# Performance work log

Measured on AMD Instinct MI355X. Metric: run time of the kernel, lower is better.

## Reference

```python
import jax, jax.numpy as jnp
import numpy as np

MODEL_DIM = 1024
NUM_HEADS = 16
HEAD_DIM = MODEL_DIM // NUM_HEADS
WINDOW = 4


def local_mask(seq_len):
    i = jnp.arange(seq_len)
    return jnp.abs(i[:, None] - i[None, :]) <= WINDOW  # [S,S] bool


def setup_inputs() -> dict:
    key = jax.random.key(0)
    ks = jax.random.split(key, 9)
    d = MODEL_DIM
    s = 0.02
    return {
        "x": jax.random.normal(ks[0], (4, 2048, d), dtype=jnp.float32),
        "Wq": jax.random.normal(ks[1], (d, d), dtype=jnp.float32) * s,
        "bq": jnp.zeros((d,), dtype=jnp.float32),
        "Wk": jax.random.normal(ks[2], (d, d), dtype=jnp.float32) * s,
        "bk": jnp.zeros((d,), dtype=jnp.float32),
        "Wv": jax.random.normal(ks[3], (d, d), dtype=jnp.float32) * s,
        "bv": jnp.zeros((d,), dtype=jnp.float32),
        "Wo": jax.random.normal(ks[4], (d, d), dtype=jnp.float32) * s,
        "bo": jnp.zeros((d,), dtype=jnp.float32),
    }


def reference(x, Wq, bq, Wk, bk, Wv, bv, Wo, bo):
    B, S, D = x.shape
    H, Hd = NUM_HEADS, HEAD_DIM
    # linear projections (torch Linear: x @ W.T + b; here W stored pre-transposed)
    q = (x @ Wq + bq).reshape(B, S, H, Hd).transpose(0, 2, 1, 3)  # [B,H,S,Hd]
    k = (x @ Wk + bk).reshape(B, S, H, Hd).transpose(0, 2, 1, 3)
    v = (x @ Wv + bv).reshape(B, S, H, Hd).transpose(0, 2, 1, 3)
    scores = jnp.einsum("bhqd,bhkd->bhqk", q, k) / jnp.sqrt(jnp.float32(Hd))
    mask = local_mask(S)[None, None]  # [1,1,S,S]
    scores = jnp.where(mask, scores, -jnp.inf)
    weights = jax.nn.softmax(scores, axis=-1)  # [B,H,S,S]
    out = jnp.einsum("bhqk,bhkd->bhqd", weights, v)
    out = out.transpose(0, 2, 1, 3).reshape(B, S, D)
    out = out @ Wo + bo
    return (out, weights)
```

## Files before the change

kernel.cpp:

```cpp
#include <hip/hip_runtime.h>


typedef __attribute__((ext_vector_type(8))) short short8;
typedef __attribute__((ext_vector_type(4))) float f32x4;

#define B_    4
#define S_    2048
#define D_    1024
#define H_    16
#define HD_   64
#define WIN_  4
#define NROW  (B_ * S_)
#define OUT0_ELEMS  ((size_t)B_ * S_ * D_)
#define WROWS (B_ * H_ * S_)
#define TOTAL_CH (67108864ull)
#define Z0_CH 37748736ull
#define Z1_CH 16777216ull
#define ZA_BASE (Z0_CH + Z1_CH)

__device__ __forceinline__ unsigned short f2bf(float f) {
  unsigned int u = __float_as_uint(f);
  u += 0x7fffu + ((u >> 16) & 1u);
  return (unsigned short)(u >> 16);
}
__device__ __forceinline__ float bf2f(unsigned short u) {
  return __uint_as_float(((unsigned int)u) << 16);
}

__device__ __forceinline__ void zstore(f32x4* __restrict__ woutv, size_t g) {
  int row = (int)(g >> 9);
  int f = (int)(g & 511);
  int s = row & (S_ - 1);
  int f0 = (s > WIN_) ? ((s - WIN_) >> 2) : 0;
  int hi = (s + WIN_ < S_ - 1) ? (s + WIN_) : (S_ - 1);
  int f1 = hi >> 2;
  if (f < f0 || f > f1) {
    f32x4 z = {0.f, 0.f, 0.f, 0.f};
    __builtin_nontemporal_store(z, woutv + g);
  }
}

__global__ __launch_bounds__(256) void xconv_k(const float* __restrict__ x,
                                               unsigned short* __restrict__ o) {
  int i = blockIdx.x * 256 + threadIdx.x;
  float4 f = reinterpret_cast<const float4*>(x)[i];
  ushort4 u;
  u.x = f2bf(f.x); u.y = f2bf(f.y); u.z = f2bf(f.z); u.w = f2bf(f.w);
  reinterpret_cast<ushort4*>(o)[i] = u;
}

__global__ __launch_bounds__(256) void wconv_k(const float* __restrict__ W0,
                                               const float* __restrict__ W1,
                                               const float* __restrict__ W2,
                                               const float* __restrict__ W3,
                                               unsigned short* __restrict__ out) {
  __shared__ float t[32][33];
  const float* Ws[4] = {W0, W1, W2, W3};
  const float* W = Ws[blockIdx.z];
  unsigned short* o = out + (size_t)blockIdx.z * D_ * D_;
  int tx = threadIdx.x;
  int ty = threadIdx.y;
  int n0 = blockIdx.x * 32, k0 = blockIdx.y * 32;
#pragma unroll
  for (int i = 0; i < 4; ++i)
    t[ty + 8 * i][tx] = W[(size_t)(k0 + ty + 8 * i) * D_ + (n0 + tx)];
  __syncthreads();
#pragma unroll
  for (int i = 0; i < 4; ++i)
    o[(size_t)(n0 + ty + 8 * i) * D_ + (k0 + tx)] = f2bf(t[tx][ty + 8 * i]);
}

#define GLD16(g, l)                                                            \
  __builtin_amdgcn_global_load_lds(                                            \
      (const __attribute__((address_space(1))) unsigned int*)(g),              \
      (__attribute__((address_space(3))) unsigned int*)(l), 16, 0, 0)

__global__ __launch_bounds__(256) void gemm_qkv_k(
    const unsigned short* __restrict__ A, const unsigned short* __restrict__ Wt,
    const float* __restrict__ bq, const float* __restrict__ bk,
    const float* __restrict__ bv, unsigned short* __restrict__ Qb,
    unsigned short* __restrict__ Kb, unsigned short* __restrict__ Vb,
    float* __restrict__ wout) {
  __shared__ unsigned short As[128 * 32];
  __shared__ unsigned short Bs[128 * 32];
  const int tid = threadIdx.x;
  const int lane = tid & 63;
  const int wid = tid >> 6;
  const int wm = wid >> 1, wn = wid & 1;
  const int row0 = blockIdx.x * 128;
  const int col0 = blockIdx.y * 128;
  f32x4* woutv = (f32x4*)wout;
  const unsigned int gt = (blockIdx.y * 64u + blockIdx.x) * 256u + tid;

  f32x4 acc[4][4] = {};
  const int frow = lane & 15;
  const int koff = (lane >> 4) << 3;

  for (int kt = 0; kt < 32; ++kt) {
#pragma unroll
    for (int i = 0; i < 2; ++i) {
      int c = tid + (i << 8);
      int r = c >> 2;
      int kk = (c & 3) << 3;
      GLD16(A + (size_t)(row0 + r) * D_ + (kt << 5) + kk, (char*)As + c * 16);
      GLD16(Wt + (size_t)(col0 + r) * D_ + (kt << 5) + kk, (char*)Bs + c * 16);
    }
#pragma unroll
    for (int j = 0; j < 3; ++j)
      zstore(woutv, (size_t)(kt * 3 + j) * 393216u + gt);
    __syncthreads();
    short8 af[4], bfr[4];
#pragma unroll
    for (int mi = 0; mi < 4; ++mi)
      af[mi] = *reinterpret_cast<const short8*>(
          &As[(wm * 64 + mi * 16 + frow) * 32 + koff]);
#pragma unroll
    for (int ni = 0; ni < 4; ++ni)
      bfr[ni] = *reinterpret_cast<const short8*>(
          &Bs[(wn * 64 + ni * 16 + frow) * 32 + koff]);
#pragma unroll
    for (int mi = 0; mi < 4; ++mi)
#pragma unroll
      for (int ni = 0; ni < 4; ++ni)
        acc[mi][ni] = __builtin_amdgcn_mfma_f32_16x16x32_bf16(
            af[mi], bfr[ni], acc[mi][ni], 0, 0, 0);
    __syncthreads();
  }

#pragma unroll
  for (int mi = 0; mi < 4; ++mi) {
#pragma unroll
    for (int ni = 0; ni < 4; ++ni) {
#pragma unroll
      for (int r = 0; r < 4; ++r) {
        int gr = row0 + wm * 64 + mi * 16 + ((lane >> 4) << 2) + r;
        int gc = col0 + wn * 64 + ni * 16 + (lane & 15);
        int z = gc >> 10;
        int ci = gc & 1023;
        float bias = (z == 0) ? bq[ci] : (z == 1) ? bk[ci] : bv[ci];
        unsigned short* outp = (z == 0) ? Qb : (z == 1) ? Kb : Vb;
        int b = gr >> 11, s = gr & (S_ - 1);
        int h = ci >> 6, hd = ci & 63;
        outp[(((size_t)(b * H_ + h) * S_ + s) << 6) + hd] =
            f2bf(acc[mi][ni][r] + bias);
      }
    }
  }
}

__global__ __launch_bounds__(256) void gemm_out_k(
    const unsigned short* __restrict__ A, const unsigned short* __restrict__ Bt,
    const float* __restrict__ bias, float* __restrict__ o,
    float* __restrict__ wout) {
  __shared__ unsigned short As[128 * 32];
  __shared__ unsigned short Bs[128 * 32];
  const int tid = threadIdx.x;
  const int lane = tid & 63;
  const int wid = tid >> 6;
  const int wm = wid >> 1, wn = wid & 1;
  const int row0 = blockIdx.x * 128;
  const int col0 = blockIdx.y * 128;
  f32x4* woutv = (f32x4*)wout;
  const unsigned int gt = (blockIdx.y * 64u + blockIdx.x) * 256u + tid;

  f32x4 acc[4][4] = {};
  const int frow = lane & 15;
  const int koff = (lane >> 4) << 3;

  for (int kt = 0; kt < 32; ++kt) {
#pragma unroll
    for (int i = 0; i < 2; ++i) {
      int c = tid + (i << 8);
      int r = c >> 2;
      int kk = (c & 3) << 3;
      GLD16(A + (size_t)(row0 + r) * D_ + (kt << 5) + kk, (char*)As + c * 16);
      GLD16(Bt + (size_t)(col0 + r) * D_ + (kt << 5) + kk, (char*)Bs + c * 16);
    }
#pragma unroll
    for (int j = 0; j < 4; ++j)
      zstore(woutv, Z0_CH + (size_t)(kt * 4 + j) * 131072u + gt);
    __syncthreads();
    short8 af[4], bfr[4];
#pragma unroll
    for (int mi = 0; mi < 4; ++mi)
      af[mi] = *reinterpret_cast<const short8*>(
          &As[(wm * 64 + mi * 16 + frow) * 32 + koff]);
#pragma unroll
    for (int ni = 0; ni < 4; ++ni)
      bfr[ni] = *reinterpret_cast<const short8*>(
          &Bs[(wn * 64 + ni * 16 + frow) * 32 + koff]);
#pragma unroll
    for (int mi = 0; mi < 4; ++mi)
#pragma unroll
      for (int ni = 0; ni < 4; ++ni)
        acc[mi][ni] = __builtin_amdgcn_mfma_f32_16x16x32_bf16(
            af[mi], bfr[ni], acc[mi][ni], 0, 0, 0);
    __syncthreads();
  }

#pragma unroll
  for (int mi = 0; mi < 4; ++mi) {
#pragma unroll
    for (int ni = 0; ni < 4; ++ni) {
#pragma unroll
      for (int r = 0; r < 4; ++r) {
        int gr = row0 + wm * 64 + mi * 16 + ((lane >> 4) << 2) + r;
        int gc = col0 + wn * 64 + ni * 16 + (lane & 15);
        o[(size_t)gr * D_ + gc] = acc[mi][ni][r] + bias[gc];
      }
    }
  }
}

__global__ __launch_bounds__(256) void attn_k(const unsigned short* __restrict__ Q,
                                              const unsigned short* __restrict__ K,
                                              const unsigned short* __restrict__ V,
                                              float* __restrict__ wout,
                                              unsigned short* __restrict__ attn) {
  int lane = threadIdx.x & 63;
  int wid = threadIdx.x >> 6;
  int row = blockIdx.x * 4 + wid;
  int s = row & (S_ - 1);
  int bh = row >> 11;
  int b = bh >> 4, h = bh & 15;
  float qd = bf2f(Q[(size_t)row * HD_ + lane]);
  const unsigned short* Kb = K + (size_t)bh * S_ * HD_;
  const unsigned short* Vb = V + (size_t)bh * S_ * HD_;

  float sc[9];
#pragma unroll
  for (int j = 0; j < 9; ++j) {
    int ks = s - WIN_ + j;
    bool ok = (ks >= 0) && (ks < S_);
    float v = ok ? qd * bf2f(Kb[(size_t)ks * HD_ + lane]) : 0.f;
#pragma unroll
    for (int off = 32; off > 0; off >>= 1) v += __shfl_xor(v, off, 64);
    sc[j] = ok ? v * 0.125f : -INFINITY;
  }
  float m = sc[0];
#pragma unroll
  for (int j = 1; j < 9; ++j) m = fmaxf(m, sc[j]);
  float w[9];
  float sum = 0.f;
#pragma unroll
  for (int j = 0; j < 9; ++j) { w[j] = __expf(sc[j] - m); sum += w[j]; }
  float inv = 1.f / sum;
#pragma unroll
  for (int j = 0; j < 9; ++j) w[j] *= inv;

  float o = 0.f;
#pragma unroll
  for (int j = 0; j < 9; ++j) {
    int ks = s - WIN_ + j;
    if (ks >= 0 && ks < S_) o += w[j] * bf2f(Vb[(size_t)ks * HD_ + lane]);
  }
  attn[((size_t)(b * S_ + s)) * D_ + h * HD_ + lane] = f2bf(o);

  const int lo = s - WIN_;
  const int hiq = (s + WIN_ < S_ - 1) ? (s + WIN_) : (S_ - 1);
  const int f0 = (s > WIN_) ? ((s - WIN_) >> 2) : 0;
  const int f1 = hiq >> 2;
  f32x4* rowp = reinterpret_cast<f32x4*>(wout + (size_t)row * S_);
  if (lane <= f1 - f0) {
    f32x4 v4;
#pragma unroll
    for (int e = 0; e < 4; ++e) {
      int d = ((f0 + lane) << 2) + e - lo;
      float val = 0.f;
#pragma unroll
      for (int j = 0; j < 9; ++j)
        if (d == j) val = w[j];
      v4[e] = val;
    }
    __builtin_nontemporal_store(v4, rowp + f0 + lane);
  }

  unsigned int gtid = blockIdx.x * 256u + threadIdx.x;
#pragma unroll
  for (int k2 = 0; k2 < 2; ++k2) {
    size_t g = ZA_BASE + (size_t)k2 * 8388608u + gtid;
    if (g < TOTAL_CH) zstore((f32x4*)wout, g);
  }
}

extern "C" void kernel_launch(void* const* d_in, const int* in_sizes, int n_in,
                              void* d_out, int out_size, void* d_ws,
                              size_t ws_size, hipStream_t stream) {
  const float* x = (const float*)d_in[0];
  const float* Wq = (const float*)d_in[1];
  const float* bq = (const float*)d_in[2];
  const float* Wk = (const float*)d_in[3];
  const float* bk = (const float*)d_in[4];
  const float* Wv = (const float*)d_in[5];
  const float* bv = (const float*)d_in[6];
  const float* Wo = (const float*)d_in[7];
  const float* bo = (const float*)d_in[8];
  float* out = (float*)d_out;
  float* wout = out + OUT0_ELEMS;

  char* ws = (char*)d_ws;
  unsigned short* x_bf = (unsigned short*)(ws);
  unsigned short* Wt = (unsigned short*)(ws + (16ull << 20));
  unsigned short* Qb = (unsigned short*)(ws + (24ull << 20));
  unsigned short* Kb = (unsigned short*)(ws + (40ull << 20));
  unsigned short* Vb = (unsigned short*)(ws + (56ull << 20));
  unsigned short* attn = (unsigned short*)(ws + (72ull << 20));

  xconv_k<<<NROW * D_ / 1024, 256, 0, stream>>>(x, x_bf);
  wconv_k<<<dim3(32, 32, 4), dim3(32, 8), 0, stream>>>(Wq, Wk, Wv, Wo, Wt);
  gemm_qkv_k<<<dim3(64, 24), 256, 0, stream>>>(x_bf, Wt, bq, bk, bv, Qb, Kb,
                                               Vb, wout);
  attn_k<<<(B_ * H_ * S_) / 4, 256, 0, stream>>>(Qb, Kb, Vb, wout, attn);
  gemm_out_k<<<dim3(64, 8), 256, 0, stream>>>(
      attn, Wt + (size_t)3 * D_ * D_, bo, out, wout);
}
```

Measured before the change: 340.9 us.

## Split mask-fill stores into dedicated blocks and remap GEMM tiles for locality

New measurement: 343.2 us. No clear change (+0.7%).

```diff
diff --git a/kernel.cpp b/kernel.cpp
--- a/kernel.cpp
+++ b/kernel.cpp
@@ -12,7 +12,6 @@
 #define WIN_  4
 #define NROW  (B_ * S_)
 #define OUT0_ELEMS  ((size_t)B_ * S_ * D_)
-#define WROWS (B_ * H_ * S_)
 #define TOTAL_CH (67108864ull)
 #define Z0_CH 37748736ull
 #define Z1_CH 16777216ull
@@ -83,14 +82,26 @@
     float* __restrict__ wout) {
   __shared__ unsigned short As[128 * 32];
   __shared__ unsigned short Bs[128 * 32];
+  const int b = blockIdx.x;
+  const int g8 = b >> 3, o = b & 7;
+
+  if ((g8 & 3) == 3) {
+    const int fb = (g8 >> 2) * 8 + o;
+    const unsigned int t0 = fb * 256u + threadIdx.x;
+    f32x4* woutv = (f32x4*)wout;
+    for (int it = 0; it < 288; ++it)
+      zstore(woutv, (size_t)it * 131072u + t0);
+    return;
+  }
+
+  const int gg = g8 - (g8 >> 2);
+  const int row0 = (o * 8 + (gg & 7)) * 128;
+  const int col0 = (gg >> 3) * 128;
+
   const int tid = threadIdx.x;
   const int lane = tid & 63;
   const int wid = tid >> 6;
   const int wm = wid >> 1, wn = wid & 1;
-  const int row0 = blockIdx.x * 128;
-  const int col0 = blockIdx.y * 128;
-  f32x4* woutv = (f32x4*)wout;
-  const unsigned int gt = (blockIdx.y * 64u + blockIdx.x) * 256u + tid;
 
   f32x4 acc[4][4] = {};
   const int frow = lane & 15;
@@ -105,9 +116,6 @@
       GLD16(A + (size_t)(row0 + r) * D_ + (kt << 5) + kk, (char*)As + c * 16);
       GLD16(Wt + (size_t)(col0 + r) * D_ + (kt << 5) + kk, (char*)Bs + c * 16);
     }
-#pragma unroll
-    for (int j = 0; j < 3; ++j)
-      zstore(woutv, (size_t)(kt * 3 + j) * 393216u + gt);
     __syncthreads();
     short8 af[4], bfr[4];
 #pragma unroll
@@ -139,9 +147,9 @@
         int ci = gc & 1023;
         float bias = (z == 0) ? bq[ci] : (z == 1) ? bk[ci] : bv[ci];
         unsigned short* outp = (z == 0) ? Qb : (z == 1) ? Kb : Vb;
-        int b = gr >> 11, s = gr & (S_ - 1);
+        int bb = gr >> 11, s = gr & (S_ - 1);
         int h = ci >> 6, hd = ci & 63;
-        outp[(((size_t)(b * H_ + h) * S_ + s) << 6) + hd] =
+        outp[(((size_t)(bb * H_ + h) * S_ + s) << 6) + hd] =
             f2bf(acc[mi][ni][r] + bias);
       }
     }
@@ -150,18 +158,30 @@
 
 __global__ __launch_bounds__(256) void gemm_out_k(
     const unsigned short* __restrict__ A, const unsigned short* __restrict__ Bt,
-    const float* __restrict__ bias, float* __restrict__ o,
+    const float* __restrict__ bias, float* __restrict__ o_,
     float* __restrict__ wout) {
   __shared__ unsigned short As[128 * 32];
   __shared__ unsigned short Bs[128 * 32];
+  const int b = blockIdx.x;
+  const int g8 = b >> 3, o = b & 7;
+
+  if (g8 % 3 == 2) {
+    const int fb = (g8 / 3) * 8 + o;
+    const unsigned int t0 = fb * 256u + threadIdx.x;
+    f32x4* woutv = (f32x4*)wout;
+    for (int it = 0; it < 256; ++it)
+      zstore(woutv, Z0_CH + (size_t)it * 65536u + t0);
+    return;
+  }
+
+  const int gg = g8 - (g8 + 1) / 3;
+  const int row0 = (o * 8 + (gg & 7)) * 128;
+  const int col0 = (gg >> 3) * 128;
+
   const int tid = threadIdx.x;
   const int lane = tid & 63;
   const int wid = tid >> 6;
   const int wm = wid >> 1, wn = wid & 1;
-  const int row0 = blockIdx.x * 128;
-  const int col0 = blockIdx.y * 128;
-  f32x4* woutv = (f32x4*)wout;
-  const unsigned int gt = (blockIdx.y * 64u + blockIdx.x) * 256u + tid;
 
   f32x4 acc[4][4] = {};
   const int frow = lane & 15;
@@ -176,9 +196,6 @@
       GLD16(A + (size_t)(row0 + r) * D_ + (kt << 5) + kk, (char*)As + c * 16);
       GLD16(Bt + (size_t)(col0 + r) * D_ + (kt << 5) + kk, (char*)Bs + c * 16);
     }
-#pragma unroll
-    for (int j = 0; j < 4; ++j)
-      zstore(woutv, Z0_CH + (size_t)(kt * 4 + j) * 131072u + gt);
     __syncthreads();
     short8 af[4], bfr[4];
 #pragma unroll
@@ -206,7 +223,7 @@
       for (int r = 0; r < 4; ++r) {
         int gr = row0 + wm * 64 + mi * 16 + ((lane >> 4) << 2) + r;
         int gc = col0 + wn * 64 + ni * 16 + (lane & 15);
-        o[(size_t)gr * D_ + gc] = acc[mi][ni][r] + bias[gc];
+        o_[(size_t)gr * D_ + gc] = acc[mi][ni][r] + bias[gc];
       }
     }
   }
@@ -308,9 +325,8 @@
 
   xconv_k<<<NROW * D_ / 1024, 256, 0, stream>>>(x, x_bf);
   wconv_k<<<dim3(32, 32, 4), dim3(32, 8), 0, stream>>>(Wq, Wk, Wv, Wo, Wt);
-  gemm_qkv_k<<<dim3(64, 24), 256, 0, stream>>>(x_bf, Wt, bq, bk, bv, Qb, Kb,
-                                               Vb, wout);
+  gemm_qkv_k<<<2048, 256, 0, stream>>>(x_bf, Wt, bq, bk, bv, Qb, Kb, Vb, wout);
   attn_k<<<(B_ * H_ * S_) / 4, 256, 0, stream>>>(Qb, Kb, Vb, wout, attn);
-  gemm_out_k<<<dim3(64, 8), 256, 0, stream>>>(
-      attn, Wt + (size_t)3 * D_ * D_, bo, out, wout);
-}
+  gemm_out_k<<<768, 256, 0, stream>>>(attn, Wt + (size_t)3 * D_ * D_, bo, out,
+                                      wout);
+}
```
